# Performance work log

Hardware: AMD Instinct MI355X
Metric: run time of the kernel (lower is better)

Reference implementation:

```python
import jax, jax.numpy as jnp
import numpy as np

ROI_SIZE = 7
CROP = ROI_SIZE * 2  # tf crop_and_resize target before 2x2 maxpool


def crop_and_resize(img, boxes, size):
    """TF-semantics bilinear crop_and_resize for a single image.
    img: [H, W, C]; boxes: [N, 4] normalized (y1, x1, y2, x2). -> [N, size, size, C]
    """
    H, W, C = img.shape
    y1, x1, y2, x2 = boxes[:, 0], boxes[:, 1], boxes[:, 2], boxes[:, 3]
    i = jnp.arange(size, dtype=boxes.dtype)
    # TF: in_y = y1*(H-1) + i*(y2-y1)*(H-1)/(size-1)
    ys = y1[:, None] * (H - 1) + i[None, :] * ((y2 - y1)[:, None] * (H - 1) / (size - 1))  # [N,S]
    xs = x1[:, None] * (W - 1) + i[None, :] * ((x2 - x1)[:, None] * (W - 1) / (size - 1))  # [N,S]
    y0 = jnp.floor(ys)
    x0 = jnp.floor(xs)
    wy = (ys - y0)[:, :, None, None]  # [N,S,1,1]
    wx = (xs - x0)[:, None, :, None]  # [N,1,S,1]
    y0i = jnp.clip(y0.astype(jnp.int32), 0, H - 1)
    y1i = jnp.clip(y0i + 1, 0, H - 1)
    x0i = jnp.clip(x0.astype(jnp.int32), 0, W - 1)
    x1i = jnp.clip(x0i + 1, 0, W - 1)

    def gather(yi, xi):  # [N,S],[N,S] -> [N,S,S,C]
        return img[yi[:, :, None], xi[:, None, :]]

    top = gather(y0i, x0i) * (1 - wx) + gather(y0i, x1i) * wx
    bot = gather(y1i, x0i) * (1 - wx) + gather(y1i, x1i) * wx
    return top * (1 - wy) + bot * wy


def setup_inputs() -> dict:
    key = jax.random.key(0)
    ks = jax.random.split(key, 10)
    feats = jax.random.uniform(ks[0], (1, 38, 50, 512), dtype=jnp.float32)  # relu-like feature map
    # valid normalized boxes: sort endpoints per axis
    yy = jnp.sort(jax.random.uniform(ks[1], (1000, 2), dtype=jnp.float32), axis=1)
    xx = jnp.sort(jax.random.uniform(ks[2], (1000, 2), dtype=jnp.float32), axis=1)
    proposals = jnp.stack([yy[:, 0], xx[:, 0], yy[:, 1], xx[:, 1]], axis=1)  # [N,4] y1,x1,y2,x2
    d_flat = ROI_SIZE * ROI_SIZE * 512  # 25088
    W1 = jax.random.normal(ks[3], (d_flat, 4096), dtype=jnp.float32) * 0.01
    b1 = jnp.zeros((4096,), jnp.float32)
    W2 = jax.random.normal(ks[4], (4096, 4096), dtype=jnp.float32) * 0.01
    b2 = jnp.zeros((4096,), jnp.float32)
    Wc = jax.random.normal(ks[5], (4096, 21), dtype=jnp.float32) * 0.01  # class head, stddev 0.01
    bc = jnp.zeros((21,), jnp.float32)
    Wr = jax.random.normal(ks[6], (4096, 80), dtype=jnp.float32) * 0.001  # reg head, stddev 0.001
    br = jnp.zeros((80,), jnp.float32)
    return {"feats": feats, "proposals": proposals, "W1": W1, "b1": b1, "W2": W2,
            "b2": b2, "Wc": Wc, "bc": bc, "Wr": Wr, "br": br}


def reference(feats, proposals, W1, b1, W2, b2, Wc, bc, Wr, br):
    # roi_pool: crop_and_resize to 14x14 (batch_idx all 0), then 2x2 maxpool stride 2 -> 7x7
    rois = crop_and_resize(feats[0], proposals, CROP)  # [N,14,14,C]
    N, _, _, C = rois.shape
    pooled = rois.reshape(N, ROI_SIZE, 2, ROI_SIZE, 2, C).max(axis=(2, 4))  # [N,7,7,C]
    x = pooled.reshape(N, -1)  # flatten (row-major, matches keras Flatten on NHWC)
    x = jax.nn.relu(x @ W1 + b1)
    x = jax.nn.relu(x @ W2 + b2)
    cls_out = jax.nn.softmax(x @ Wc + bc, axis=-1)          # [N, num_classes]
    reg_out = (x @ Wr + br).reshape(N, -1, 4)               # [N, num_classes-1, 4]
    return cls_out, reg_out
```

## Files before the change

kernel.cpp:

```cpp
#include <hip/hip_runtime.h>
#include <stdint.h>

typedef __bf16 bf16x8 __attribute__((ext_vector_type(8)));
typedef float f32x16 __attribute__((ext_vector_type(16)));

__device__ __forceinline__ unsigned short f2bf(float f) {
    unsigned int u = __float_as_uint(f);
    unsigned int r = (u + 0x7fffu + ((u >> 16) & 1u)) >> 16;
    return (unsigned short)r;
}
__device__ __forceinline__ float bf2f(unsigned int h) {
    return __uint_as_float(h << 16);
}

__device__ __forceinline__ void gld_lds16(const void* g, void* l) {
    __builtin_amdgcn_global_load_lds((const __attribute__((address_space(1))) void*)g,
                                     (__attribute__((address_space(3))) void*)l, 16, 0, 0);
}

__global__ __launch_bounds__(256) void k_cvt_feats(const float* __restrict__ src,
                                                   unsigned short* __restrict__ dst) {
    int g = blockIdx.x * 256 + threadIdx.x;
    float4 v = ((const float4*)src)[g];
    ushort4 o;
    o.x = f2bf(v.x); o.y = f2bf(v.y); o.z = f2bf(v.z); o.w = f2bf(v.w);
    ((ushort4*)dst)[g] = o;
}

__global__ __launch_bounds__(256) void k_roipool(const unsigned short* __restrict__ feats,
                                                 const float* __restrict__ props,
                                                 unsigned short* __restrict__ pooled) {
    int b = blockIdx.x;
    int r = b / 49;
    int cell = b - r * 49;
    int py = cell / 7, px = cell - py * 7;
    int c = threadIdx.x * 2;
    unsigned int* outp = (unsigned int*)(pooled + (size_t)r * 25088 + cell * 512 + c);
    if (r >= 1000) { *outp = 0u; return; }
    float y1 = props[r * 4 + 0], x1 = props[r * 4 + 1];
    float y2 = props[r * 4 + 2], x2 = props[r * 4 + 3];
    float sy = (y2 - y1) * (37.0f / 13.0f);
    float sx = (x2 - x1) * (49.0f / 13.0f);
    float m0 = -1e30f, m1 = -1e30f;
#pragma unroll
    for (int a = 0; a < 2; ++a) {
        float ys = y1 * 37.0f + (float)(2 * py + a) * sy;
        float y0f = floorf(ys);
        float wy = ys - y0f;
        int y0 = (int)y0f; y0 = min(max(y0, 0), 37);
        int y1i = min(y0 + 1, 37);
#pragma unroll
        for (int bb = 0; bb < 2; ++bb) {
            float xs = x1 * 49.0f + (float)(2 * px + bb) * sx;
            float x0f = floorf(xs);
            float wx = xs - x0f;
            int x0 = (int)x0f; x0 = min(max(x0, 0), 49);
            int x1i = min(x0 + 1, 49);
            unsigned int t00 = *(const unsigned int*)(feats + ((y0 * 50 + x0) * 512 + c));
            unsigned int t01 = *(const unsigned int*)(feats + ((y0 * 50 + x1i) * 512 + c));
            unsigned int t10 = *(const unsigned int*)(feats + ((y1i * 50 + x0) * 512 + c));
            unsigned int t11 = *(const unsigned int*)(feats + ((y1i * 50 + x1i) * 512 + c));
            float w00 = (1.f - wy) * (1.f - wx), w01 = (1.f - wy) * wx;
            float w10 = wy * (1.f - wx), w11 = wy * wx;
            float v0 = bf2f(t00 & 0xffffu) * w00 + bf2f(t01 & 0xffffu) * w01 +
                       bf2f(t10 & 0xffffu) * w10 + bf2f(t11 & 0xffffu) * w11;
            float v1 = bf2f(t00 >> 16) * w00 + bf2f(t01 >> 16) * w01 +
                       bf2f(t10 >> 16) * w10 + bf2f(t11 >> 16) * w11;
            m0 = fmaxf(m0, v0);
            m1 = fmaxf(m1, v1);
        }
    }
    *outp = ((unsigned int)f2bf(m1) << 16) | (unsigned int)f2bf(m0);
}

__global__ __launch_bounds__(256) void k_transpose_cvt(const float* __restrict__ B,
                                                       unsigned short* __restrict__ BT,
                                                       int K, int N) {
    __shared__ unsigned int tile[64][32];
    int k0 = blockIdx.x * 64;
    int n0 = blockIdx.y * 64;
    int t = threadIdx.x;
    int kr = (t >> 4) * 2;
    int c4 = (t & 15) * 4;
#pragma unroll
    for (int ii = 0; ii < 2; ++ii) {
        int k = kr + ii * 32;
        int kd = k >> 1;
        const float* p0 = B + (size_t)(k0 + k) * N + n0 + c4;
        float4 v0 = *(const float4*)p0;
        float4 v1 = *(const float4*)(p0 + N);
        float lo[4] = {v0.x, v0.y, v0.z, v0.w};
        float hi[4] = {v1.x, v1.y, v1.z, v1.w};
#pragma unroll
        for (int c = 0; c < 4; ++c) {
            int n = c4 + c;
            int dw = (((kd >> 1) ^ ((n >> 2) & 7)) << 1) | (kd & 1);
            tile[n][dw] = (unsigned)f2bf(lo[c]) | ((unsigned)f2bf(hi[c]) << 16);
        }
    }
    __syncthreads();
    int nl = t >> 2;
    int x = (nl >> 2) & 7;
    int pbase = (t & 3) * 4;
    uint2 r[4];
#pragma unroll
    for (int q = 0; q < 4; ++q) {
        int p = (pbase + q) ^ x;
        r[q] = *(const uint2*)&tile[nl][p << 1];
    }
    unsigned short* dst = BT + (size_t)(n0 + nl) * K + k0 + (t & 3) * 16;
    uint4 o0, o1;
    o0.x = r[0].x; o0.y = r[0].y; o0.z = r[1].x; o0.w = r[1].y;
    o1.x = r[2].x; o1.y = r[2].y; o1.z = r[3].x; o1.w = r[3].y;
    *(uint4*)(dst + 0) = o0;
    *(uint4*)(dst + 8) = o1;
}

__global__ __launch_bounds__(256) void k_gemm(const unsigned short* __restrict__ A,
                                              const unsigned short* __restrict__ BT,
                                              float* __restrict__ Cpart,
                                              int N, int K, int kChunk, int MN) {
    __shared__ __align__(16) unsigned short As[128 * 64];
    __shared__ __align__(16) unsigned short Bs[128 * 64];
    const int n0 = blockIdx.x * 128;
    const int m0 = blockIdx.y * 128;
    const int kBeg = blockIdx.z * kChunk;
    const int kEnd = kBeg + kChunk;
    const int t = threadIdx.x;
    const int lane = t & 63;
    const int wave = t >> 6;
    const int wm = (wave & 1) * 64;
    const int wn = (wave >> 1) * 64;
    const int l31 = lane & 31;
    const int half = lane >> 5;
    const int xorb = l31 & 7;

    const int srow = t >> 3;
    const int sj = (t & 7) ^ (srow & 7);
    const unsigned short* ag = A + (size_t)(m0 + srow) * K + sj * 8;
    const unsigned short* bg = BT + (size_t)(n0 + srow) * K + sj * 8;
    char* alb = (char*)As + t * 16;
    char* blb = (char*)Bs + t * 16;
    const int rq = K * 32;

    f32x16 acc[2][2] = {};
    const unsigned short* aBase = As + (wm + l31) * 64;
    const unsigned short* bBase = Bs + (wn + l31) * 64;

    for (int kt = kBeg; kt < kEnd; kt += 64) {
#pragma unroll
        for (int q = 0; q < 4; ++q) gld_lds16(ag + kt + q * rq, alb + q * 4096);
#pragma unroll
        for (int q = 0; q < 4; ++q) gld_lds16(bg + kt + q * rq, blb + q * 4096);
        __syncthreads();
#pragma unroll
        for (int s = 0; s < 4; ++s) {
            const int off = ((s * 2 + half) ^ xorb) * 8;
            bf16x8 a0 = *(const bf16x8*)(aBase + off);
            bf16x8 a1 = *(const bf16x8*)(aBase + 2048 + off);
            bf16x8 b0 = *(const bf16x8*)(bBase + off);
            bf16x8 b1 = *(const bf16x8*)(bBase + 2048 + off);
            acc[0][0] = __builtin_amdgcn_mfma_f32_32x32x16_bf16(a0, b0, acc[0][0], 0, 0, 0);
            acc[0][1] = __builtin_amdgcn_mfma_f32_32x32x16_bf16(a0, b1, acc[0][1], 0, 0, 0);
            acc[1][0] = __builtin_amdgcn_mfma_f32_32x32x16_bf16(a1, b0, acc[1][0], 0, 0, 0);
            acc[1][1] = __builtin_amdgcn_mfma_f32_32x32x16_bf16(a1, b1, acc[1][1], 0, 0, 0);
        }
        __syncthreads();
    }

    float* Cp = Cpart + (size_t)blockIdx.z * MN;
    const int colb = n0 + wn + l31;
    const int rbase = m0 + wm + 4 * half;
#pragma unroll
    for (int i = 0; i < 2; ++i)
#pragma unroll
        for (int j = 0; j < 2; ++j)
#pragma unroll
            for (int reg = 0; reg < 16; ++reg) {
                int row = rbase + i * 32 + (reg & 3) + 8 * (reg >> 2);
                Cp[(size_t)row * N + colb + j * 32] = acc[i][j][reg];
            }
}

__global__ __launch_bounds__(256) void k_bias_relu_cvt(const float* __restrict__ accP,
                                                       const float* __restrict__ bias,
                                                       unsigned short* __restrict__ out) {
    int gI = blockIdx.x * 256 + threadIdx.x;
    const float4* p = (const float4*)accP;
    float4 v0 = p[gI];
    float4 v1 = p[gI + 1048576];
    float4 v2 = p[gI + 2097152];
    float4 v3 = p[gI + 3145728];
    float4 b = ((const float4*)bias)[gI & 1023];
    ushort4 o;
    o.x = f2bf(fmaxf(v0.x + v1.x + v2.x + v3.x + b.x, 0.f));
    o.y = f2bf(fmaxf(v0.y + v1.y + v2.y + v3.y + b.y, 0.f));
    o.z = f2bf(fmaxf(v0.z + v1.z + v2.z + v3.z + b.z, 0.f));
    o.w = f2bf(fmaxf(v0.w + v1.w + v2.w + v3.w + b.w, 0.f));
    ((ushort4*)out)[gI] = o;
}

__global__ __launch_bounds__(256) void k_pack_w3(const float* __restrict__ Wc,
                                                 const float* __restrict__ Wr,
                                                 unsigned short* __restrict__ W3T) {
    int gI = blockIdx.x * 256 + threadIdx.x;
    int n = gI >> 12, k = gI & 4095;
    float v = 0.f;
    if (n < 21) v = Wc[k * 21 + n];
    else if (n < 101) v = Wr[k * 80 + (n - 21)];
    W3T[gI] = f2bf(v);
}

__global__ __launch_bounds__(64) void k_head(const float* __restrict__ acc3,
                                             const float* __restrict__ bc,
                                             const float* __restrict__ br,
                                             float* __restrict__ out) {
    int r = blockIdx.x;
    int lane = threadIdx.x;
    float logit = -1e30f;
    if (lane < 21) {
        logit = bc[lane];
#pragma unroll
        for (int z = 0; z < 16; ++z) logit += acc3[z * 131072 + r * 128 + lane];
    }
    float mx = logit;
#pragma unroll
    for (int m = 32; m >= 1; m >>= 1) mx = fmaxf(mx, __shfl_xor(mx, m, 64));
    float e = (lane < 21) ? expf(logit - mx) : 0.f;
    float s = e;
#pragma unroll
    for (int m = 32; m >= 1; m >>= 1) s += __shfl_xor(s, m, 64);
    if (lane < 21) out[r * 21 + lane] = e / s;
    for (int j = lane; j < 80; j += 64) {
        float v = br[j];
#pragma unroll
        for (int z = 0; z < 16; ++z) v += acc3[z * 131072 + r * 128 + 21 + j];
        out[21000 + r * 80 + j] = v;
    }
}

extern "C" void kernel_launch(void* const* d_in, const int* in_sizes, int n_in,
                              void* d_out, int out_size, void* d_ws, size_t ws_size,
                              hipStream_t stream) {
    (void)in_sizes; (void)n_in; (void)out_size; (void)ws_size;
    const float* feats = (const float*)d_in[0];
    const float* props = (const float*)d_in[1];
    const float* W1    = (const float*)d_in[2];
    const float* b1    = (const float*)d_in[3];
    const float* W2    = (const float*)d_in[4];
    const float* b2    = (const float*)d_in[5];
    const float* Wc    = (const float*)d_in[6];
    const float* bc    = (const float*)d_in[7];
    const float* Wr    = (const float*)d_in[8];
    const float* br    = (const float*)d_in[9];
    float* out = (float*)d_out;

    char* ws = (char*)d_ws;
    unsigned short* W1T    = (unsigned short*)ws; ws += (size_t)4096 * 25088 * 2;
    unsigned short* W2T    = (unsigned short*)ws; ws += (size_t)4096 * 4096 * 2;
    unsigned short* W3T    = (unsigned short*)ws; ws += (size_t)128 * 4096 * 2;
    unsigned short* featsb = (unsigned short*)ws; ws += (size_t)972800 * 2;
    unsigned short* pooled = (unsigned short*)ws; ws += (size_t)1024 * 25088 * 2;
    unsigned short* x1     = (unsigned short*)ws; ws += (size_t)1024 * 4096 * 2;
    unsigned short* x2     = (unsigned short*)ws; ws += (size_t)1024 * 4096 * 2;
    float* accP            = (float*)ws;          ws += (size_t)4 * 1024 * 4096 * 4;
    float* acc3P           = accP;

    k_cvt_feats<<<950, 256, 0, stream>>>(feats, featsb);
    k_roipool<<<1024 * 49, 256, 0, stream>>>(featsb, props, pooled);
    k_transpose_cvt<<<dim3(392, 64), 256, 0, stream>>>(W1, W1T, 25088, 4096);
    k_gemm<<<dim3(32, 8, 4), 256, 0, stream>>>(pooled, W1T, accP, 4096, 25088, 6272, 1024 * 4096);
    k_bias_relu_cvt<<<4096, 256, 0, stream>>>(accP, b1, x1);
    k_transpose_cvt<<<dim3(64, 64), 256, 0, stream>>>(W2, W2T, 4096, 4096);
    k_gemm<<<dim3(32, 8, 4), 256, 0, stream>>>(x1, W2T, accP, 4096, 4096, 1024, 1024 * 4096);
    k_bias_relu_cvt<<<4096, 256, 0, stream>>>(accP, b2, x2);
    k_pack_w3<<<2048, 256, 0, stream>>>(Wc, Wr, W3T);
    k_gemm<<<dim3(1, 8, 16), 256, 0, stream>>>(x2, W3T, acc3P, 128, 4096, 256, 1024 * 128);
    k_head<<<1000, 64, 0, stream>>>(acc3P, bc, br, out);
}
```

Baseline: 1.024 ms.

## Add 256x256-tile 512-thread GEMM with double-buffered LDS for FC1/FC2

Adds a new GEMM kernel using 256x256 output tiles, 8 waves, 16x16x32 bf16 MFMA and a 128KB double-buffered LDS pipeline that stages A and B tiles via direct global-to-LDS loads interleaved with compute. It replaces the 128x128 kernel for the two large fully connected layers. Each staged tile now feeds more MFMA work, which cuts global and LDS traffic per flop. The split-K launch drops to 256 blocks, so fewer workgroups are resident per CU and the large LDS footprint limits occupancy.

```diff
diff --git a/kernel.cpp b/kernel.cpp
--- a/kernel.cpp
+++ b/kernel.cpp
@@ -3,6 +3,7 @@
 
 typedef __bf16 bf16x8 __attribute__((ext_vector_type(8)));
 typedef float f32x16 __attribute__((ext_vector_type(16)));
+typedef float f32x4 __attribute__((ext_vector_type(4)));
 
 __device__ __forceinline__ unsigned short f2bf(float f) {
     unsigned int u = __float_as_uint(f);
@@ -116,6 +117,127 @@
     *(uint4*)(dst + 8) = o1;
 }
 
+__global__ __launch_bounds__(512, 2) void k_gemm256(const unsigned short* __restrict__ A,
+                                                    const unsigned short* __restrict__ BT,
+                                                    float* __restrict__ Cpart,
+                                                    int N, int K, int kChunk, int MN) {
+    __shared__ __align__(16) char lds[131072];
+    const int n0 = blockIdx.x * 256;
+    const int m0 = blockIdx.y * 256;
+    const int kBeg = blockIdx.z * kChunk;
+    const int NT = kChunk >> 6;
+    const int t = threadIdx.x;
+    const int l = t & 63;
+    const int wave = t >> 6;
+    const int wrow = wave >> 2;
+    const int wcol = wave & 3;
+    const int l15 = l & 15;
+    const int lq = l >> 4;
+    const size_t rK = (size_t)K;
+
+    const int rowoff = l15 * 128;
+    const int cb0 = ((lq ^ (l & 7)) << 4);
+    const int cb1 = (((4 + lq) ^ (l & 7)) << 4);
+
+    const int srow = t >> 3;
+    const int sj = (t & 7) ^ (srow & 7);
+    const unsigned short* agp = A + (size_t)(m0 + srow) * rK + sj * 8;
+    const unsigned short* bgp = BT + (size_t)(n0 + srow) * rK + sj * 8;
+    char* aldst = (char*)lds + t * 16;
+    char* bldst = (char*)lds + 32768 + t * 16;
+
+#define STAGE_A(bi, h, kt) do {                                                           \
+        gld_lds16(agp + (size_t)((h) * 128) * rK + (kt), aldst + (bi) * 65536 + (h) * 16384);        \
+        gld_lds16(agp + (size_t)((h) * 128 + 64) * rK + (kt), aldst + (bi) * 65536 + (h) * 16384 + 8192); \
+    } while (0)
+#define STAGE_B(bi, h, kt) do {                                                           \
+        gld_lds16(bgp + (size_t)((h) * 128) * rK + (kt), bldst + (bi) * 65536 + (h) * 16384);        \
+        gld_lds16(bgp + (size_t)((h) * 128 + 64) * rK + (kt), bldst + (bi) * 65536 + (h) * 16384 + 8192); \
+    } while (0)
+
+    f32x4 acc[8][4];
+#pragma unroll
+    for (int i = 0; i < 8; ++i)
+#pragma unroll
+        for (int j = 0; j < 4; ++j) acc[i][j] = (f32x4){0.f, 0.f, 0.f, 0.f};
+
+    bf16x8 bB[4][2];
+    bf16x8 aA[2][2];
+
+    STAGE_A(0, 0, kBeg); STAGE_A(0, 1, kBeg);
+    STAGE_B(0, 0, kBeg); STAGE_B(0, 1, kBeg);
+    STAGE_B(1, 0, kBeg + 64); STAGE_B(1, 1, kBeg + 64);
+    asm volatile("s_waitcnt vmcnt(4)" ::: "memory");
+    __builtin_amdgcn_s_barrier();
+
+    int cur = 0;
+    for (int tt = 0; tt < NT; ++tt) {
+        const char* Ab = (const char*)lds + cur * 65536 + wrow * 16384 + rowoff;
+        const char* Bb = (const char*)lds + cur * 65536 + 32768 + wcol * 8192 + rowoff;
+        const int nx = cur ^ 1;
+        const bool tn1 = (tt + 1 < NT);
+        const bool tn2 = (tt + 2 < NT);
+        const int k1 = kBeg + (tt + 1) * 64;
+        const int k2 = kBeg + (tt + 2) * 64;
+#pragma unroll
+        for (int q = 0; q < 4; ++q) {
+            aA[0][0] = *(const bf16x8*)(Ab + (2 * q) * 2048 + cb0);
+            aA[0][1] = *(const bf16x8*)(Ab + (2 * q) * 2048 + cb1);
+            aA[1][0] = *(const bf16x8*)(Ab + (2 * q + 1) * 2048 + cb0);
+            aA[1][1] = *(const bf16x8*)(Ab + (2 * q + 1) * 2048 + cb1);
+            if (q == 0) {
+#pragma unroll
+                for (int nf = 0; nf < 4; ++nf) {
+                    bB[nf][0] = *(const bf16x8*)(Bb + nf * 2048 + cb0);
+                    bB[nf][1] = *(const bf16x8*)(Bb + nf * 2048 + cb1);
+                }
+            }
+            if (q == 0) { if (tn1) STAGE_A(nx, 0, k1); }
+            if (q == 1) { if (tn1) STAGE_A(nx, 1, k1); }
+            if (q == 2) { if (tn2) STAGE_B(cur, 0, k2); }
+            if (q == 3) {
+                if (tn2) {
+                    STAGE_B(cur, 1, k2);
+                    asm volatile("s_waitcnt vmcnt(4)" ::: "memory");
+                } else {
+                    asm volatile("s_waitcnt vmcnt(0)" ::: "memory");
+                }
+            }
+            __builtin_amdgcn_s_barrier();
+            asm volatile("s_waitcnt lgkmcnt(0)" ::: "memory");
+            __builtin_amdgcn_s_setprio(1);
+#pragma unroll
+            for (int kh = 0; kh < 2; ++kh)
+#pragma unroll
+                for (int nf = 0; nf < 4; ++nf) {
+                    acc[2 * q][nf] = __builtin_amdgcn_mfma_f32_16x16x32_bf16(
+                        aA[0][kh], bB[nf][kh], acc[2 * q][nf], 0, 0, 0);
+                    acc[2 * q + 1][nf] = __builtin_amdgcn_mfma_f32_16x16x32_bf16(
+                        aA[1][kh], bB[nf][kh], acc[2 * q + 1][nf], 0, 0, 0);
+                }
+            __builtin_amdgcn_s_setprio(0);
+            __builtin_amdgcn_s_barrier();
+        }
+        cur = nx;
+    }
+#undef STAGE_A
+#undef STAGE_B
+
+    float* Cp = Cpart + (size_t)blockIdx.z * MN;
+    const int row0 = m0 + wrow * 128 + lq * 4;
+    const int col0 = n0 + wcol * 64 + l15;
+#pragma unroll
+    for (int mf = 0; mf < 8; ++mf)
+#pragma unroll
+        for (int r = 0; r < 4; ++r) {
+            float* p = Cp + (size_t)(row0 + mf * 16 + r) * N + col0;
+            p[0]  = acc[mf][0][r];
+            p[16] = acc[mf][1][r];
+            p[32] = acc[mf][2][r];
+            p[48] = acc[mf][3][r];
+        }
+}
+
 __global__ __launch_bounds__(256) void k_gemm(const unsigned short* __restrict__ A,
                                               const unsigned short* __restrict__ BT,
                                               float* __restrict__ Cpart,
@@ -269,10 +391,10 @@
     k_cvt_feats<<<950, 256, 0, stream>>>(feats, featsb);
     k_roipool<<<1024 * 49, 256, 0, stream>>>(featsb, props, pooled);
     k_transpose_cvt<<<dim3(392, 64), 256, 0, stream>>>(W1, W1T, 25088, 4096);
-    k_gemm<<<dim3(32, 8, 4), 256, 0, stream>>>(pooled, W1T, accP, 4096, 25088, 6272, 1024 * 4096);
+    k_gemm256<<<dim3(16, 4, 4), 512, 0, stream>>>(pooled, W1T, accP, 4096, 25088, 6272, 1024 * 4096);
     k_bias_relu_cvt<<<4096, 256, 0, stream>>>(accP, b1, x1);
     k_transpose_cvt<<<dim3(64, 64), 256, 0, stream>>>(W2, W2T, 4096, 4096);
-    k_gemm<<<dim3(32, 8, 4), 256, 0, stream>>>(x1, W2T, accP, 4096, 4096, 1024, 1024 * 4096);
+    k_gemm256<<<dim3(16, 4, 4), 512, 0, stream>>>(x1, W2T, accP, 4096, 4096, 1024, 1024 * 4096);
     k_bias_relu_cvt<<<4096, 256, 0, stream>>>(accP, b2, x2);
     k_pack_w3<<<2048, 256, 0, stream>>>(Wc, Wr, W3T);
     k_gemm<<<dim3(1, 8, 16), 256, 0, stream>>>(x2, W3T, acc3P, 128, 4096, 256, 1024 * 128);
```

Result: faster. 932.0 us (-9.0%).
